# Kernel tuning notes

Hardware: AMD Instinct MI355X
Metric: run time of the kernel (lower is better)

The kernel has to match this reference:

```python
import jax, jax.numpy as jnp
import numpy as np

B, T, C, H, D, E, K = 4, 1024, 1024, 16, 64, 8, 2
HID = 2 * D  # expert MLP hidden width (assumed 2*head_dim)
NEG = jnp.finfo(jnp.float32).min


def setup_inputs() -> dict:
    key = jax.random.key(0)
    ks = jax.random.split(key, 16)
    s = 0.02
    # rotary tables [max_pos, head_dim]
    inv_freq = 1.0 / (10000.0 ** (jnp.arange(0, D, 2, dtype=jnp.float32) / D))
    freqs = jnp.arange(T, dtype=jnp.float32)[:, None] * inv_freq[None, :]
    emb = jnp.concatenate([freqs, freqs], axis=-1)  # [T, D]
    return {
        "x": jax.random.normal(ks[0], (B, T, C), jnp.float32),
        "position_ids": jnp.sort(jax.random.randint(ks[1], (B, T), 0, T), axis=-1),
        "cos": jnp.cos(emb),
        "sin": jnp.sin(emb),
        "rq": s * jax.random.normal(ks[2], (D, E), jnp.float32),
        "rk": s * jax.random.normal(ks[3], (D, E), jnp.float32),
        "rv": s * jax.random.normal(ks[4], (D, E), jnp.float32),
        "q_w1": s * jax.random.normal(ks[5], (E, D, HID), jnp.float32),
        "q_w2": s * jax.random.normal(ks[6], (E, HID, D), jnp.float32),
        "k_w1": s * jax.random.normal(ks[7], (E, D, HID), jnp.float32),
        "k_w2": s * jax.random.normal(ks[8], (E, HID, D), jnp.float32),
        "v_w1": s * jax.random.normal(ks[9], (E, D, HID), jnp.float32),
        "v_w2": s * jax.random.normal(ks[10], (E, HID, D), jnp.float32),
        "o_w": s * jax.random.normal(ks[11], (C, C), jnp.float32),  # torch Linear weight [out,in]
    }


def _rotate_half(x):
    x1, x2 = x[..., : D // 2], x[..., D // 2:]
    return jnp.concatenate([-x2, x1], axis=-1)


def _moe_head_proj(xh, r_w, w1, w2):
    """Per-head top-k routed expert MLP. xh: [B,T,H,D]."""
    logits = jnp.einsum('bthd,de->bthe', xh, r_w)            # router logits
    vals, idx = jax.lax.top_k(logits, K)                     # [B,T,H,K]
    w = jax.nn.softmax(vals, axis=-1)
    onehot = jax.nn.one_hot(idx, E, dtype=xh.dtype)          # [B,T,H,K,E]
    w_full = jnp.einsum('bthk,bthke->bthe', w, onehot)       # scatter weights to all experts
    h = jax.nn.gelu(jnp.einsum('bthd,edf->bthef', xh, w1))   # all-expert hidden
    out = jnp.einsum('bthe,bthef,efg->bthg', w_full, h, w2)  # masked weighted combine
    return out, logits


def reference(x, position_ids, cos, sin, rq, rk, rv, q_w1, q_w2, k_w1, k_w2, v_w1, v_w2, o_w):
    xh = x.reshape(B, T, H, D)
    q, _ = _moe_head_proj(xh, rq, q_w1, q_w2)
    k, _ = _moe_head_proj(xh, rk, k_w1, k_w2)
    v, _ = _moe_head_proj(xh, rv, v_w1, v_w2)
    q = q.transpose(0, 2, 1, 3)  # [B,H,T,D]
    k = k.transpose(0, 2, 1, 3)
    v = v.transpose(0, 2, 1, 3)
    # RoPE
    c = cos[position_ids][:, None, :, :]  # [B,1,T,D]
    s = sin[position_ids][:, None, :, :]
    q = q * c + _rotate_half(q) * s
    k = k * c + _rotate_half(k) * s
    # causal SDPA
    scores = jnp.einsum('bhqd,bhkd->bhqk', q, k) / jnp.sqrt(jnp.float32(D))
    causal = jnp.tril(jnp.ones((T, T), dtype=bool))
    scores = jnp.where(causal, scores, NEG)
    attn = jax.nn.softmax(scores, axis=-1)
    out = jnp.einsum('bhqk,bhkd->bhqd', attn, v)
    out = out.transpose(0, 2, 1, 3).reshape(B, T, C)
    return out @ o_w.T
```

## Files before the change

kernel.cpp:

```cpp
#include <hip/hip_runtime.h>
#include <math.h>

#define BB 4
#define TT 1024
#define CCH 1024
#define HH 16
#define DD 64
#define EE 8
#define HID 128
#define CAP 8192
#define GEXP 252

typedef unsigned short u16;
typedef short bf16x8 __attribute__((ext_vector_type(8)));
typedef float f32x4 __attribute__((ext_vector_type(4)));

__device__ __forceinline__ u16 f2bf(float f) {
    unsigned int u = __float_as_uint(f);
    unsigned int r = (u + 0x7FFFu + ((u >> 16) & 1u)) >> 16;
    return (u16)r;
}
__device__ __forceinline__ u16 f2bf_f(float f) {
    return (u16)((__float_as_uint(f) + 0x8000u) >> 16);
}
__device__ __forceinline__ float gelu_fast(float z) {
    float t = z * z;
    float wn = __builtin_fmaf(t, -0.07135481283f, -1.5957691216f);
    float e = __expf(z * wn);
    return __fdividef(z, 1.f + e);
}

__global__ __launch_bounds__(256) void router_kernel(
    const float* __restrict__ x,
    const float* __restrict__ rq, const float* __restrict__ rk, const float* __restrict__ rv,
    unsigned int* __restrict__ counts,
    unsigned int* __restrict__ idxbuf, float2* __restrict__ wtbuf)
{
    const int tid = threadIdx.x;
    const unsigned int g = blockIdx.x * 256 + tid;

    __shared__ float rS[3][64][8];
    __shared__ int lcnt[192];
    __shared__ int lbase[192];

    for (int i = tid; i < 1536; i += 256) {
        int p = i >> 9, rem = i & 511;
        const float* rp = (p == 0) ? rq : (p == 1) ? rk : rv;
        rS[p][rem >> 3][rem & 7] = rp[rem];
    }
    if (tid < 192) lcnt[tid] = 0;
    __syncthreads();

    float lg[3][8];
    #pragma unroll
    for (int p = 0; p < 3; ++p)
        #pragma unroll
        for (int e = 0; e < 8; ++e) lg[p][e] = 0.f;

    const float* xr = x + (size_t)g * 64;
    for (int i4 = 0; i4 < 16; ++i4) {
        float4 xv = ((const float4*)xr)[i4];
        float xa[4] = {xv.x, xv.y, xv.z, xv.w};
        #pragma unroll
        for (int m = 0; m < 4; ++m) {
            int d = i4 * 4 + m;
            #pragma unroll
            for (int p = 0; p < 3; ++p) {
                float4 r0 = *(const float4*)&rS[p][d][0];
                float4 r1 = *(const float4*)&rS[p][d][4];
                lg[p][0] += xa[m] * r0.x; lg[p][1] += xa[m] * r0.y;
                lg[p][2] += xa[m] * r0.z; lg[p][3] += xa[m] * r0.w;
                lg[p][4] += xa[m] * r1.x; lg[p][5] += xa[m] * r1.y;
                lg[p][6] += xa[m] * r1.z; lg[p][7] += xa[m] * r1.w;
            }
        }
    }

    int ppe[3]; float2 pw[3]; int slot[3];
    #pragma unroll
    for (int p = 0; p < 3; ++p) {
        int i1 = 0; float v1 = lg[p][0];
        #pragma unroll
        for (int e = 1; e < 8; ++e) { if (lg[p][e] > v1) { v1 = lg[p][e]; i1 = e; } }
        int i2 = -1; float v2 = -3.402823466e38f;
        #pragma unroll
        for (int e = 0; e < 8; ++e) { if (e != i1 && lg[p][e] > v2) { v2 = lg[p][e]; i2 = e; } }
        float z = __expf(v2 - v1);
        float inv = 1.f / (1.f + z);
        float wa = inv, wb = z * inv;
        int lo = min(i1, i2), hi = max(i1, i2);
        float wlo = (i1 < i2) ? wa : wb;
        float whi = (i1 < i2) ? wb : wa;
        int pel = p * 64 + lo * 8 + hi;
        ppe[p] = pel; pw[p] = make_float2(wlo, whi);
        slot[p] = atomicAdd(&lcnt[pel], 1);
    }
    __syncthreads();
    if (tid < 192) {
        int c = lcnt[tid];
        lbase[tid] = c ? (int)atomicAdd(&counts[tid], (unsigned int)c) : 0;
    }
    __syncthreads();
    #pragma unroll
    for (int p = 0; p < 3; ++p) {
        int pos = lbase[ppe[p]] + slot[p];
        if (pos < CAP) {
            idxbuf[ppe[p] * CAP + pos] = g;
            wtbuf[ppe[p] * CAP + pos]  = pw[p];
        }
    }
}

__global__ __launch_bounds__(128) void sched_kernel(
    const unsigned int* __restrict__ counts, unsigned int* __restrict__ blockinfo)
{
    const int tid = threadIdx.x;
    __shared__ int nsub[84];
    __shared__ int extra[84];
    __shared__ int frac[84];
    __shared__ int alloc[84];
    __shared__ int startS[84];
    __shared__ int nnzS, totalS, rem2S;

    if (tid < 84) {
        int p = tid / 28, q = tid - 28 * p, lo = 0;
        while (q >= 7 - lo) { q -= 7 - lo; ++lo; }
        int hi = lo + 1 + q;
        int n = (int)counts[p * 64 + lo * 8 + hi];
        if (n > CAP) n = CAP;
        nsub[tid] = (n + 31) >> 5;
    }
    __syncthreads();
    if (tid == 0) {
        int tot = 0, nz = 0;
        for (int i = 0; i < 84; ++i) { tot += nsub[i]; nz += (nsub[i] > 0); }
        totalS = tot; nnzS = nz;
    }
    __syncthreads();
    const int R = GEXP - nnzS;
    if (tid < 84) {
        if (nsub[tid] > 0) {
            int e = (int)(((long long)nsub[tid] * R) / totalS);
            extra[tid] = e;
            frac[tid] = nsub[tid] * R - e * totalS;
        } else { extra[tid] = 0; frac[tid] = -1; }
    }
    __syncthreads();
    if (tid == 0) {
        int se = 0;
        for (int i = 0; i < 84; ++i) se += extra[i];
        rem2S = GEXP - nnzS - se;
    }
    __syncthreads();
    if (tid < 84) {
        if (nsub[tid] > 0) {
            int rank = 0;
            for (int j = 0; j < 84; ++j)
                if (nsub[j] > 0 && (frac[j] > frac[tid] || (frac[j] == frac[tid] && j < tid))) ++rank;
            alloc[tid] = 1 + extra[tid] + (rank < rem2S ? 1 : 0);
        } else alloc[tid] = 0;
    }
    __syncthreads();
    if (tid == 0) {
        int s = 0;
        for (int i = 0; i < 84; ++i) { startS[i] = s; s += alloc[i]; }
    }
    __syncthreads();
    if (tid < 84) {
        int a = alloc[tid], st = startS[tid];
        for (int c = 0; c < a; ++c)
            blockinfo[st + c] = (unsigned)tid | ((unsigned)c << 8) | ((unsigned)a << 20);
    }
}

__global__ __launch_bounds__(768) void expert_kernel(
    const float* __restrict__ x, const int* __restrict__ pos_ids,
    const float* __restrict__ cosb, const float* __restrict__ sinb,
    const float* __restrict__ w1q, const float* __restrict__ w2q,
    const float* __restrict__ w1k, const float* __restrict__ w2k,
    const float* __restrict__ w1v, const float* __restrict__ w2v,
    const unsigned int* __restrict__ counts,
    const unsigned int* __restrict__ idxbuf, const float2* __restrict__ wtbuf,
    const unsigned int* __restrict__ blockinfo,
    u16* __restrict__ qb, u16* __restrict__ kb, u16* __restrict__ vb)
{
    const int tid = threadIdx.x;
    const unsigned int info = blockinfo[blockIdx.x];
    const int pe84 = info & 255;
    const int chunk = (info >> 8) & 0xFFF;
    const int nch = info >> 20;
    const int p = pe84 / 28;
    int q28 = pe84 - p * 28;
    int lo = 0;
    while (q28 >= 7 - lo) { q28 -= 7 - lo; ++lo; }
    const int hi = lo + 1 + q28;
    const int pe = p * 64 + lo * 8 + hi;

    int n = (int)counts[pe]; if (n == 0) return; if (n > CAP) n = CAP;

    const float* w1base = (p == 0) ? w1q : (p == 1) ? w1k : w1v;
    const float* w2base = (p == 0) ? w2q : (p == 1) ? w2k : w2v;
    u16* outp = (p == 0) ? qb : (p == 1) ? kb : vb;
    const unsigned int* il = idxbuf + pe * CAP;
    const float2* wl = wtbuf + pe * CAP;

    __shared__ u16 w1t[2][128][72];
    __shared__ u16 w2t[2][64][136];
    __shared__ u16 hsw[12][32][40];

    #pragma unroll
    for (int e = 0; e < 2; ++e) {
        int ex = e ? hi : lo;
        const float* w1 = w1base + ex * 64 * 128;
        const float* w2 = w2base + ex * 128 * 64;
        for (int i = tid; i < 8192; i += 768)
            w1t[e][i & 127][i >> 7] = f2bf(w1[i]);
        for (int i = tid; i < 8192; i += 768)
            w2t[e][i & 63][i >> 6] = f2bf(w2[i]);
    }
    __syncthreads();

    const int lane = tid & 63, w = tid >> 6, quad = lane >> 4, m16 = lane & 15;
    const int wid = chunk * 12 + w;
    const int WRK = nch * 12;
    const int nsub = (n + 31) >> 5;

    for (int s = wid; s < nsub; s += WRK) {
        const int base = s * 32;
        unsigned int gtok = 0, obase = 0; float wlo_ = 0.f, whi_ = 0.f;
        int posv = 0, valid = 0;
        if (lane < 32) {
            int j = base + lane;
            valid = (j < n);
            int jc = valid ? j : (n - 1);
            gtok = il[jc];
            float2 wv = wl[jc];
            wlo_ = valid ? wv.x : 0.f; whi_ = valid ? wv.y : 0.f;
            unsigned int b_ = gtok >> 14, h_ = gtok & 15, t_ = (gtok >> 4) & 1023;
            obase = ((b_ * 16 + h_) * 1024 + t_) * 64;
            posv = pos_ids[b_ * 1024 + t_];
        }

        bf16x8 Afr[2][2];
        #pragma unroll
        for (int mt2 = 0; mt2 < 2; ++mt2) {
            unsigned int gm = (unsigned int)__shfl((int)gtok, mt2 * 16 + m16, 64);
            const float* xr = x + (size_t)gm * 64 + 8 * quad;
            float4 xa0 = *(const float4*)(xr);
            float4 xa1 = *(const float4*)(xr + 4);
            float4 xb0 = *(const float4*)(xr + 32);
            float4 xb1 = *(const float4*)(xr + 36);
            bf16x8 A0, A1;
            A0[0] = (short)f2bf_f(xa0.x); A0[1] = (short)f2bf_f(xa0.y);
            A0[2] = (short)f2bf_f(xa0.z); A0[3] = (short)f2bf_f(xa0.w);
            A0[4] = (short)f2bf_f(xa1.x); A0[5] = (short)f2bf_f(xa1.y);
            A0[6] = (short)f2bf_f(xa1.z); A0[7] = (short)f2bf_f(xa1.w);
            A1[0] = (short)f2bf_f(xb0.x); A1[1] = (short)f2bf_f(xb0.y);
            A1[2] = (short)f2bf_f(xb0.z); A1[3] = (short)f2bf_f(xb0.w);
            A1[4] = (short)f2bf_f(xb1.x); A1[5] = (short)f2bf_f(xb1.y);
            A1[6] = (short)f2bf_f(xb1.z); A1[7] = (short)f2bf_f(xb1.w);
            Afr[mt2][0] = A0; Afr[mt2][1] = A1;
        }

        f32x4 acc2[2][2][4];
        #pragma unroll
        for (int e = 0; e < 2; ++e)
            #pragma unroll
            for (int mt2 = 0; mt2 < 2; ++mt2)
                #pragma unroll
                for (int nt = 0; nt < 4; ++nt) acc2[e][mt2][nt] = (f32x4){0.f, 0.f, 0.f, 0.f};

        #pragma unroll
        for (int e = 0; e < 2; ++e) {
            #pragma unroll
            for (int kk = 0; kk < 4; ++kk) {
                int nt0 = 2 * kk, nt1 = 2 * kk + 1;
                bf16x8 b0a = *(const bf16x8*)&w1t[e][16 * nt0 + m16][8 * quad];
                bf16x8 b0b = *(const bf16x8*)&w1t[e][16 * nt0 + m16][32 + 8 * quad];
                bf16x8 b1a = *(const bf16x8*)&w1t[e][16 * nt1 + m16][8 * quad];
                bf16x8 b1b = *(const bf16x8*)&w1t[e][16 * nt1 + m16][32 + 8 * quad];
                #pragma unroll
                for (int mt2 = 0; mt2 < 2; ++mt2) {
                    f32x4 c0 = (f32x4){0.f, 0.f, 0.f, 0.f};
                    f32x4 c1 = (f32x4){0.f, 0.f, 0.f, 0.f};
                    c0 = __builtin_amdgcn_mfma_f32_16x16x32_bf16(Afr[mt2][0], b0a, c0, 0, 0, 0);
                    c0 = __builtin_amdgcn_mfma_f32_16x16x32_bf16(Afr[mt2][1], b0b, c0, 0, 0, 0);
                    c1 = __builtin_amdgcn_mfma_f32_16x16x32_bf16(Afr[mt2][0], b1a, c1, 0, 0, 0);
                    c1 = __builtin_amdgcn_mfma_f32_16x16x32_bf16(Afr[mt2][1], b1b, c1, 0, 0, 0);
                    #pragma unroll
                    for (int r = 0; r < 4; ++r) {
                        hsw[w][mt2 * 16 + 4 * quad + r][m16]      = f2bf_f(gelu_fast(c0[r]));
                        hsw[w][mt2 * 16 + 4 * quad + r][16 + m16] = f2bf_f(gelu_fast(c1[r]));
                    }
                }
                bf16x8 A2_0 = *(const bf16x8*)&hsw[w][m16][8 * quad];
                bf16x8 A2_1 = *(const bf16x8*)&hsw[w][16 + m16][8 * quad];
                #pragma unroll
                for (int nt2 = 0; nt2 < 4; ++nt2) {
                    bf16x8 b2 = *(const bf16x8*)&w2t[e][16 * nt2 + m16][32 * kk + 8 * quad];
                    acc2[e][0][nt2] = __builtin_amdgcn_mfma_f32_16x16x32_bf16(A2_0, b2, acc2[e][0][nt2], 0, 0, 0);
                    acc2[e][1][nt2] = __builtin_amdgcn_mfma_f32_16x16x32_bf16(A2_1, b2, acc2[e][1][nt2], 0, 0, 0);
                }
            }
        }

        #pragma unroll
        for (int mt2 = 0; mt2 < 2; ++mt2) {
            #pragma unroll
            for (int r = 0; r < 4; ++r) {
                int tk = mt2 * 16 + 4 * quad + r;
                float wlo_r = __shfl(wlo_, tk, 64);
                float whi_r = __shfl(whi_, tk, 64);
                int   pos_r = __shfl(posv, tk, 64);
                unsigned int ob = (unsigned int)__shfl((int)obase, tk, 64);
                int   val_r = __shfl(valid, tk, 64);
                if (p < 2) {
                    #pragma unroll
                    for (int ntp = 0; ntp < 2; ++ntp) {
                        int d = 16 * ntp + m16;
                        float v1 = wlo_r * acc2[0][mt2][ntp][r]     + whi_r * acc2[1][mt2][ntp][r];
                        float v2 = wlo_r * acc2[0][mt2][ntp + 2][r] + whi_r * acc2[1][mt2][ntp + 2][r];
                        float cd = cosb[pos_r * 64 + d];
                        float sd = sinb[pos_r * 64 + d];
                        if (val_r) {
                            outp[ob + d]      = f2bf(v1 * cd - v2 * sd);
                            outp[ob + d + 32] = f2bf(v2 * cd + v1 * sd);
                        }
                    }
                } else {
                    #pragma unroll
                    for (int nt = 0; nt < 4; ++nt) {
                        float v = wlo_r * acc2[0][mt2][nt][r] + whi_r * acc2[1][mt2][nt][r];
                        if (val_r) outp[ob + 16 * nt + m16] = f2bf(v);
                    }
                }
            }
        }
    }
}

__global__ __launch_bounds__(256) void cvt_bf16_kernel(
    const float* __restrict__ in, u16* __restrict__ out, int n4)
{
    int i = blockIdx.x * 256 + threadIdx.x;
    if (i >= n4) return;
    float4 v = ((const float4*)in)[i];
    unsigned int lov = (unsigned int)f2bf(v.x) | ((unsigned int)f2bf(v.y) << 16);
    unsigned int hiv = (unsigned int)f2bf(v.z) | ((unsigned int)f2bf(v.w) << 16);
    ((uint2*)out)[i] = make_uint2(lov, hiv);
}

__global__ __launch_bounds__(256) void attn_kernel(
    const u16* __restrict__ qbp, const u16* __restrict__ kbp,
    const u16* __restrict__ vbp, u16* __restrict__ ao)
{
    const int tid = threadIdx.x;
    const int i8 = blockIdx.x & 7;
    const int plane_i = blockIdx.x >> 3;
    const int h = plane_i & 15, b = plane_i >> 4;
    const size_t plane = (size_t)plane_i * 1024 * 64;
    const u16* qp = qbp + plane;
    const u16* kp = kbp + plane;
    const u16* vp = vbp + plane;

    const int w = tid >> 6, lane = tid & 63, quad = lane >> 4, m16 = lane & 15;
    const int row = tid >> 2, seg = tid & 3;
    const int kjv = tid & 63, dgv = tid >> 6;

    __shared__ u16 Ks[64][72];
    __shared__ u16 Vt[64][72];
    __shared__ u16 Ps[4][16][72];

    #pragma unroll 1
    for (int half = 0; half < 2; ++half) {
        const int qt = half ? (15 - i8) : i8;
        const int q0 = qt * 64;

        const u16* qrow = &qp[(size_t)(q0 + 16 * w + m16) * 64 + 8 * quad];
        bf16x8 aq0 = *(const bf16x8*)(qrow);
        bf16x8 aq1 = *(const bf16x8*)(qrow + 32);

        uint4 kr0, kr1; ushort4 vr0, vr1, vr2, vr3;
        {
            const uint4* src = (const uint4*)&kp[(size_t)row * 64 + seg * 16];
            kr0 = src[0]; kr1 = src[1];
            const u16* vb2 = &vp[(size_t)kjv * 64 + dgv * 4];
            vr0 = *(const ushort4*)(vb2);
            vr1 = *(const ushort4*)(vb2 + 16);
            vr2 = *(const ushort4*)(vb2 + 32);
            vr3 = *(const ushort4*)(vb2 + 48);
        }

        float m_r[4], l_r[4];
        #pragma unroll
        for (int i = 0; i < 4; ++i) { m_r[i] = -1e30f; l_r[i] = 0.f; }
        f32x4 oacc[4];
        #pragma unroll
        for (int i = 0; i < 4; ++i) oacc[i] = (f32x4){0.f, 0.f, 0.f, 0.f};

        for (int kt = 0; kt <= qt; ++kt) {
            __syncthreads();
            {
                uint4* dst = (uint4*)&Ks[row][seg * 16];
                dst[0] = kr0; dst[1] = kr1;
                int d0 = dgv * 4;
                Vt[d0 + 0][kjv] = vr0.x; Vt[d0 + 1][kjv] = vr0.y;
                Vt[d0 + 2][kjv] = vr0.z; Vt[d0 + 3][kjv] = vr0.w;
                Vt[d0 + 16][kjv] = vr1.x; Vt[d0 + 17][kjv] = vr1.y;
                Vt[d0 + 18][kjv] = vr1.z; Vt[d0 + 19][kjv] = vr1.w;
                Vt[d0 + 32][kjv] = vr2.x; Vt[d0 + 33][kjv] = vr2.y;
                Vt[d0 + 34][kjv] = vr2.z; Vt[d0 + 35][kjv] = vr2.w;
                Vt[d0 + 48][kjv] = vr3.x; Vt[d0 + 49][kjv] = vr3.y;
                Vt[d0 + 50][kjv] = vr3.z; Vt[d0 + 51][kjv] = vr3.w;
            }
            __syncthreads();
            if (kt < qt) {
                const int k0n = (kt + 1) * 64;
                const uint4* src = (const uint4*)&kp[(size_t)(k0n + row) * 64 + seg * 16];
                kr0 = src[0]; kr1 = src[1];
                const u16* vb2 = &vp[(size_t)(k0n + kjv) * 64 + dgv * 4];
                vr0 = *(const ushort4*)(vb2);
                vr1 = *(const ushort4*)(vb2 + 16);
                vr2 = *(const ushort4*)(vb2 + 32);
                vr3 = *(const ushort4*)(vb2 + 48);
            }

            f32x4 sv[4];
            #pragma unroll
            for (int ct = 0; ct < 4; ++ct) {
                bf16x8 bk0 = *(const bf16x8*)&Ks[16 * ct + m16][8 * quad];
                bf16x8 bk1 = *(const bf16x8*)&Ks[16 * ct + m16][32 + 8 * quad];
                f32x4 acc = (f32x4){0.f, 0.f, 0.f, 0.f};
                acc = __builtin_amdgcn_mfma_f32_16x16x32_bf16(aq0, bk0, acc, 0, 0, 0);
                acc = __builtin_amdgcn_mfma_f32_16x16x32_bf16(aq1, bk1, acc, 0, 0, 0);
                sv[ct] = acc;
            }

            float s[4][4];
            const bool diag = (kt == qt);
            #pragma unroll
            for (int ct = 0; ct < 4; ++ct)
                #pragma unroll
                for (int reg = 0; reg < 4; ++reg) {
                    float v = sv[ct][reg] * 0.125f;
                    if (diag) {
                        int col = 16 * ct + m16;
                        int rw = 16 * w + 4 * quad + reg;
                        if (col > rw) v = -1e30f;
                    }
                    s[ct][reg] = v;
                }

            float nm[4], al[4];
            #pragma unroll
            for (int reg = 0; reg < 4; ++reg) {
                float rm = fmaxf(fmaxf(s[0][reg], s[1][reg]), fmaxf(s[2][reg], s[3][reg]));
                #pragma unroll
                for (int off = 1; off < 16; off <<= 1) rm = fmaxf(rm, __shfl_xor(rm, off, 16));
                float mn = fmaxf(m_r[reg], rm);
                nm[reg] = mn;
                al[reg] = __expf(m_r[reg] - mn);
            }
            #pragma unroll
            for (int reg = 0; reg < 4; ++reg) {
                float sum = 0.f;
                #pragma unroll
                for (int ct = 0; ct < 4; ++ct) {
                    float pv = __expf(s[ct][reg] - nm[reg]);
                    s[ct][reg] = pv;
                    sum += pv;
                }
                #pragma unroll
                for (int off = 1; off < 16; off <<= 1) sum += __shfl_xor(sum, off, 16);
                l_r[reg] = l_r[reg] * al[reg] + sum;
                m_r[reg] = nm[reg];
            }

            #pragma unroll
            for (int ct = 0; ct < 4; ++ct)
                #pragma unroll
                for (int reg = 0; reg < 4; ++reg)
                    Ps[w][4 * quad + reg][16 * ct + m16] = f2bf(s[ct][reg]);

            #pragma unroll
            for (int dt = 0; dt < 4; ++dt)
                #pragma unroll
                for (int reg = 0; reg < 4; ++reg) oacc[dt][reg] *= al[reg];

            bf16x8 ap0 = *(const bf16x8*)&Ps[w][m16][8 * quad];
            bf16x8 ap1 = *(const bf16x8*)&Ps[w][m16][32 + 8 * quad];
            #pragma unroll
            for (int dt = 0; dt < 4; ++dt) {
                bf16x8 bv0 = *(const bf16x8*)&Vt[16 * dt + m16][8 * quad];
                bf16x8 bv1 = *(const bf16x8*)&Vt[16 * dt + m16][32 + 8 * quad];
                oacc[dt] = __builtin_amdgcn_mfma_f32_16x16x32_bf16(ap0, bv0, oacc[dt], 0, 0, 0);
                oacc[dt] = __builtin_amdgcn_mfma_f32_16x16x32_bf16(ap1, bv1, oacc[dt], 0, 0, 0);
            }
        }

        #pragma unroll
        for (int reg = 0; reg < 4; ++reg) {
            float linv = 1.f / l_r[reg];
            int rw = q0 + 16 * w + 4 * quad + reg;
            size_t base = ((size_t)(b * 1024) + rw) * 1024 + h * 64;
            #pragma unroll
            for (int dt = 0; dt < 4; ++dt)
                ao[base + 16 * dt + m16] = f2bf(oacc[dt][reg] * linv);
        }
    }
}

__global__ __launch_bounds__(256) void oproj_kernel(
    const u16* __restrict__ A, const u16* __restrict__ Bw,
    float* __restrict__ out)
{
    const int tid = threadIdx.x;
    const int bn = blockIdx.x & 7;
    const int bm = blockIdx.x >> 3;
    const int m0 = bm * 128, n0 = bn * 128;
    const int w = tid >> 6, lane = tid & 63, quad = lane >> 4, m16 = lane & 15;
    const int wm = (w >> 1) * 64, wn = (w & 1) * 64;

    __shared__ u16 As[128][32];
    __shared__ u16 Bs[128][32];

    f32x4 acc[4][4];
    #pragma unroll
    for (int mt = 0; mt < 4; ++mt)
        #pragma unroll
        for (int nt = 0; nt < 4; ++nt) acc[mt][nt] = (f32x4){0.f, 0.f, 0.f, 0.f};

    for (int k0 = 0; k0 < 1024; k0 += 32) {
        __syncthreads();
        {
            int rw = tid >> 1, sg = (tid & 1) * 16;
            const uint4* srcA = (const uint4*)&A[(size_t)(m0 + rw) * 1024 + k0 + sg];
            uint4 a0 = srcA[0], a1 = srcA[1];
            uint4* dstA = (uint4*)&As[rw][sg];
            dstA[0] = a0; dstA[1] = a1;
            const uint4* srcB = (const uint4*)&Bw[(size_t)(n0 + rw) * 1024 + k0 + sg];
            uint4 b0 = srcB[0], b1 = srcB[1];
            uint4* dstB = (uint4*)&Bs[rw][sg];
            dstB[0] = b0; dstB[1] = b1;
        }
        __syncthreads();
        bf16x8 af[4], bf_[4];
        #pragma unroll
        for (int mt = 0; mt < 4; ++mt) af[mt] = *(const bf16x8*)&As[wm + 16 * mt + m16][8 * quad];
        #pragma unroll
        for (int nt = 0; nt < 4; ++nt) bf_[nt] = *(const bf16x8*)&Bs[wn + 16 * nt + m16][8 * quad];
        #pragma unroll
        for (int mt = 0; mt < 4; ++mt)
            #pragma unroll
            for (int nt = 0; nt < 4; ++nt)
                acc[mt][nt] = __builtin_amdgcn_mfma_f32_16x16x32_bf16(af[mt], bf_[nt], acc[mt][nt], 0, 0, 0);
    }
    #pragma unroll
    for (int mt = 0; mt < 4; ++mt)
        #pragma unroll
        for (int nt = 0; nt < 4; ++nt)
            #pragma unroll
            for (int reg = 0; reg < 4; ++reg)
                out[(size_t)(m0 + wm + 16 * mt + 4 * quad + reg) * 1024 + n0 + wn + 16 * nt + m16] =
                    acc[mt][nt][reg];
}

extern "C" void kernel_launch(void* const* d_in, const int* in_sizes, int n_in,
                              void* d_out, int out_size, void* d_ws, size_t ws_size,
                              hipStream_t stream) {
    (void)in_sizes; (void)n_in; (void)out_size; (void)ws_size;
    const float* x    = (const float*)d_in[0];
    const int*   pid  = (const int*)  d_in[1];
    const float* cosb = (const float*)d_in[2];
    const float* sinb = (const float*)d_in[3];
    const float* rq   = (const float*)d_in[4];
    const float* rk   = (const float*)d_in[5];
    const float* rv   = (const float*)d_in[6];
    const float* qw1  = (const float*)d_in[7];
    const float* qw2  = (const float*)d_in[8];
    const float* kw1  = (const float*)d_in[9];
    const float* kw2  = (const float*)d_in[10];
    const float* vw1  = (const float*)d_in[11];
    const float* vw2  = (const float*)d_in[12];
    const float* ow   = (const float*)d_in[13];
    float* out = (float*)d_out;

    const size_t MB = 1u << 20;
    char* wsb = (char*)d_ws;
    u16* qb   = (u16*)(wsb + 0 * MB);
    u16* kb   = (u16*)(wsb + 8 * MB);
    u16* vb   = (u16*)(wsb + 16 * MB);
    u16* aobf = (u16*)(wsb + 24 * MB);
    u16* owbf = (u16*)(wsb + 32 * MB);
    unsigned int* idxbuf = (unsigned int*)(wsb + 34 * MB);
    float2*       wtbuf  = (float2*)(wsb + 41 * MB);
    unsigned int* counts = (unsigned int*)(wsb + 54 * MB);
    unsigned int* blockinfo = (unsigned int*)(wsb + 54 * MB + 4096);

    hipMemsetAsync(counts, 0, 1024, stream);

    hipLaunchKernelGGL(router_kernel, dim3(256), dim3(256), 0, stream,
                       x, rq, rk, rv, counts, idxbuf, wtbuf);
    hipLaunchKernelGGL(sched_kernel, dim3(1), dim3(128), 0, stream,
                       counts, blockinfo);
    hipLaunchKernelGGL(cvt_bf16_kernel, dim3(1024), dim3(256), 0, stream,
                       ow, owbf, 1024 * 1024 / 4);
    hipLaunchKernelGGL(expert_kernel, dim3(GEXP), dim3(768), 0, stream,
                       x, pid, cosb, sinb, qw1, qw2, kw1, kw2, vw1, vw2,
                       counts, idxbuf, wtbuf, blockinfo, qb, kb, vb);
    hipLaunchKernelGGL(attn_kernel, dim3(512), dim3(256), 0, stream,
                       qb, kb, vb, aobf);
    hipLaunchKernelGGL(oproj_kernel, dim3(256), dim3(256), 0, stream,
                       aobf, owbf, out);
}
```

Baseline: 257.0 us.

## Pre-swizzle bf16 expert weights and keep MoE hidden activations in registers

A new kernel converts the expert W1/W2 weights once into XOR-swizzled bf16 images. The expert kernel then copies them straight into LDS with global_load_lds instead of doing a per-block fp32 convert and transpose. The GELU hidden tile now moves between the two MFMA stages through lane shuffles instead of an LDS round trip. Routing weights are folded into the hidden activations so both experts share one accumulator set. Block size drops to 512 threads and the grid doubles, which adds one extra kernel launch and makes the result depend on the scheduler's handling of the larger grid.

```diff
diff --git a/kernel.cpp b/kernel.cpp
--- a/kernel.cpp
+++ b/kernel.cpp
@@ -9,9 +9,10 @@
 #define EE 8
 #define HID 128
 #define CAP 8192
-#define GEXP 252
+#define GEXP 504
 
 typedef unsigned short u16;
+typedef unsigned int u32;
 typedef short bf16x8 __attribute__((ext_vector_type(8)));
 typedef float f32x4 __attribute__((ext_vector_type(4)));
 
@@ -22,6 +23,11 @@
 }
 __device__ __forceinline__ u16 f2bf_f(float f) {
     return (u16)((__float_as_uint(f) + 0x8000u) >> 16);
+}
+__device__ __forceinline__ u32 pkbf(float lo, float hi) {
+    u32 a = __float_as_uint(lo) + 0x8000u;
+    u32 b = __float_as_uint(hi) + 0x8000u;
+    return __builtin_amdgcn_perm(b, a, 0x07060302u);
 }
 __device__ __forceinline__ float gelu_fast(float z) {
     float t = z * z;
@@ -29,6 +35,10 @@
     float e = __expf(z * wn);
     return __fdividef(z, 1.f + e);
 }
+
+#define GLD16(gp, lp) __builtin_amdgcn_global_load_lds( \
+    (const __attribute__((address_space(1))) u32*)(gp), \
+    (__attribute__((address_space(3))) u32*)(lp), 16, 0, 0)
 
 __global__ __launch_bounds__(256) void router_kernel(
     const float* __restrict__ x,
@@ -173,12 +183,45 @@
     }
 }
 
-__global__ __launch_bounds__(768) void expert_kernel(
+__global__ __launch_bounds__(256) void wcvt_kernel(
+    const float* __restrict__ qw1, const float* __restrict__ kw1, const float* __restrict__ vw1,
+    const float* __restrict__ qw2, const float* __restrict__ kw2, const float* __restrict__ vw2,
+    u16* __restrict__ img1, u16* __restrict__ img2)
+{
+    int t = blockIdx.x * 256 + threadIdx.x;
+    u16 tmp[8];
+    if (t < 24576) {
+        int c = t & 7, f = (t >> 3) & 127, e = (t >> 10) & 7, p = t >> 13;
+        const float* w1 = ((p == 0) ? qw1 : (p == 1) ? kw1 : vw1) + e * 8192;
+        int dbase = 8 * (c ^ (f & 7));
+        #pragma unroll
+        for (int j = 0; j < 8; ++j) tmp[j] = f2bf(w1[(dbase + j) * 128 + f]);
+        uint4 ov;
+        ov.x = (u32)tmp[0] | ((u32)tmp[1] << 16);
+        ov.y = (u32)tmp[2] | ((u32)tmp[3] << 16);
+        ov.z = (u32)tmp[4] | ((u32)tmp[5] << 16);
+        ov.w = (u32)tmp[6] | ((u32)tmp[7] << 16);
+        ((uint4*)img1)[t] = ov;
+    } else {
+        int i = t - 24576;
+        int c = i & 15, g = (i >> 4) & 63, e = (i >> 10) & 7, p = i >> 13;
+        const float* w2 = ((p == 0) ? qw2 : (p == 1) ? kw2 : vw2) + e * 8192;
+        int fbase = 8 * (c ^ (g & 15));
+        #pragma unroll
+        for (int j = 0; j < 8; ++j) tmp[j] = f2bf(w2[(fbase + j) * 64 + g]);
+        uint4 ov;
+        ov.x = (u32)tmp[0] | ((u32)tmp[1] << 16);
+        ov.y = (u32)tmp[2] | ((u32)tmp[3] << 16);
+        ov.z = (u32)tmp[4] | ((u32)tmp[5] << 16);
+        ov.w = (u32)tmp[6] | ((u32)tmp[7] << 16);
+        ((uint4*)img2)[i] = ov;
+    }
+}
+
+__global__ __launch_bounds__(512, 4) void expert_kernel(
     const float* __restrict__ x, const int* __restrict__ pos_ids,
     const float* __restrict__ cosb, const float* __restrict__ sinb,
-    const float* __restrict__ w1q, const float* __restrict__ w2q,
-    const float* __restrict__ w1k, const float* __restrict__ w2k,
-    const float* __restrict__ w1v, const float* __restrict__ w2v,
+    const u16* __restrict__ img1, const u16* __restrict__ img2,
     const unsigned int* __restrict__ counts,
     const unsigned int* __restrict__ idxbuf, const float2* __restrict__ wtbuf,
     const unsigned int* __restrict__ blockinfo,
@@ -198,31 +241,34 @@
 
     int n = (int)counts[pe]; if (n == 0) return; if (n > CAP) n = CAP;
 
-    const float* w1base = (p == 0) ? w1q : (p == 1) ? w1k : w1v;
-    const float* w2base = (p == 0) ? w2q : (p == 1) ? w2k : w2v;
     u16* outp = (p == 0) ? qb : (p == 1) ? kb : vb;
     const unsigned int* il = idxbuf + pe * CAP;
     const float2* wl = wtbuf + pe * CAP;
 
-    __shared__ u16 w1t[2][128][72];
-    __shared__ u16 w2t[2][64][136];
-    __shared__ u16 hsw[12][32][40];
-
-    #pragma unroll
-    for (int e = 0; e < 2; ++e) {
-        int ex = e ? hi : lo;
-        const float* w1 = w1base + ex * 64 * 128;
-        const float* w2 = w2base + ex * 128 * 64;
-        for (int i = tid; i < 8192; i += 768)
-            w1t[e][i & 127][i >> 7] = f2bf(w1[i]);
-        for (int i = tid; i < 8192; i += 768)
-            w2t[e][i & 63][i >> 6] = f2bf(w2[i]);
+    __shared__ __align__(16) u16 wsh[32768];
+
+    {
+        const u16* a0 = img1 + (p * 8 + lo) * 8192;
+        const u16* b0 = img2 + (p * 8 + lo) * 8192;
+        const u16* a1 = img1 + (p * 8 + hi) * 8192;
+        const u16* b1 = img2 + (p * 8 + hi) * 8192;
+        #pragma unroll
+        for (int k = 0; k < 2; ++k) {
+            int o = (k * 512 + tid) * 8;
+            GLD16(a0 + o, wsh + o);
+            GLD16(b0 + o, wsh + 8192 + o);
+            GLD16(a1 + o, wsh + 16384 + o);
+            GLD16(b1 + o, wsh + 24576 + o);
+        }
     }
     __syncthreads();
 
     const int lane = tid & 63, w = tid >> 6, quad = lane >> 4, m16 = lane & 15;
-    const int wid = chunk * 12 + w;
-    const int WRK = nch * 12;
+    const int f7 = m16 & 7;
+    const int sA = m16 + ((quad & 1) << 5);
+    const int sB = sA + 16;
+    const int wid = chunk * 8 + w;
+    const int WRK = nch * 8;
     const int nsub = (n + 31) >> 5;
 
     for (int s = wid; s < nsub; s += WRK) {
@@ -240,6 +286,11 @@
             obase = ((b_ * 16 + h_) * 1024 + t_) * 64;
             posv = pos_ids[b_ * 1024 + t_];
         }
+
+        float wf00 = __shfl(wlo_, m16, 64);
+        float wf10 = __shfl(whi_, m16, 64);
+        float wf01 = __shfl(wlo_, 16 + m16, 64);
+        float wf11 = __shfl(whi_, 16 + m16, 64);
 
         bf16x8 Afr[2][2];
         #pragma unroll
@@ -262,44 +313,71 @@
             Afr[mt2][0] = A0; Afr[mt2][1] = A1;
         }
 
-        f32x4 acc2[2][2][4];
-        #pragma unroll
-        for (int e = 0; e < 2; ++e)
-            #pragma unroll
-            for (int mt2 = 0; mt2 < 2; ++mt2)
-                #pragma unroll
-                for (int nt = 0; nt < 4; ++nt) acc2[e][mt2][nt] = (f32x4){0.f, 0.f, 0.f, 0.f};
+        f32x4 acc2[2][4];
+        #pragma unroll
+        for (int mt2 = 0; mt2 < 2; ++mt2)
+            #pragma unroll
+            for (int nt = 0; nt < 4; ++nt) acc2[mt2][nt] = (f32x4){0.f, 0.f, 0.f, 0.f};
 
         #pragma unroll
         for (int e = 0; e < 2; ++e) {
+            const u16* w1b = wsh + e * 16384;
+            const u16* w2b = w1b + 8192;
+            const float wt0 = e ? wf10 : wf00;
+            const float wt1 = e ? wf11 : wf01;
             #pragma unroll
             for (int kk = 0; kk < 4; ++kk) {
-                int nt0 = 2 * kk, nt1 = 2 * kk + 1;
-                bf16x8 b0a = *(const bf16x8*)&w1t[e][16 * nt0 + m16][8 * quad];
-                bf16x8 b0b = *(const bf16x8*)&w1t[e][16 * nt0 + m16][32 + 8 * quad];
-                bf16x8 b1a = *(const bf16x8*)&w1t[e][16 * nt1 + m16][8 * quad];
-                bf16x8 b1b = *(const bf16x8*)&w1t[e][16 * nt1 + m16][32 + 8 * quad];
-                #pragma unroll
-                for (int mt2 = 0; mt2 < 2; ++mt2) {
-                    f32x4 c0 = (f32x4){0.f, 0.f, 0.f, 0.f};
-                    f32x4 c1 = (f32x4){0.f, 0.f, 0.f, 0.f};
-                    c0 = __builtin_amdgcn_mfma_f32_16x16x32_bf16(Afr[mt2][0], b0a, c0, 0, 0, 0);
-                    c0 = __builtin_amdgcn_mfma_f32_16x16x32_bf16(Afr[mt2][1], b0b, c0, 0, 0, 0);
-                    c1 = __builtin_amdgcn_mfma_f32_16x16x32_bf16(Afr[mt2][0], b1a, c1, 0, 0, 0);
-                    c1 = __builtin_amdgcn_mfma_f32_16x16x32_bf16(Afr[mt2][1], b1b, c1, 0, 0, 0);
+                f32x4 c[2][2];
+                #pragma unroll
+                for (int ntl = 0; ntl < 2; ++ntl) {
+                    const int f = 16 * (2 * kk + ntl) + m16;
+                    const u16* w1f = w1b + f * 64;
+                    bf16x8 wa = *(const bf16x8*)(w1f + (((quad    ) ^ f7) << 3));
+                    bf16x8 wb = *(const bf16x8*)(w1f + (((quad + 4) ^ f7) << 3));
                     #pragma unroll
-                    for (int r = 0; r < 4; ++r) {
-                        hsw[w][mt2 * 16 + 4 * quad + r][m16]      = f2bf_f(gelu_fast(c0[r]));
-                        hsw[w][mt2 * 16 + 4 * quad + r][16 + m16] = f2bf_f(gelu_fast(c1[r]));
+                    for (int mt2 = 0; mt2 < 2; ++mt2) {
+                        f32x4 t = (f32x4){0.f, 0.f, 0.f, 0.f};
+                        t = __builtin_amdgcn_mfma_f32_16x16x32_bf16(wa, Afr[mt2][0], t, 0, 0, 0);
+                        c[ntl][mt2] = __builtin_amdgcn_mfma_f32_16x16x32_bf16(wb, Afr[mt2][1], t, 0, 0, 0);
                     }
                 }
-                bf16x8 A2_0 = *(const bf16x8*)&hsw[w][m16][8 * quad];
-                bf16x8 A2_1 = *(const bf16x8*)&hsw[w][16 + m16][8 * quad];
-                #pragma unroll
-                for (int nt2 = 0; nt2 < 4; ++nt2) {
-                    bf16x8 b2 = *(const bf16x8*)&w2t[e][16 * nt2 + m16][32 * kk + 8 * quad];
-                    acc2[e][0][nt2] = __builtin_amdgcn_mfma_f32_16x16x32_bf16(A2_0, b2, acc2[e][0][nt2], 0, 0, 0);
-                    acc2[e][1][nt2] = __builtin_amdgcn_mfma_f32_16x16x32_bf16(A2_1, b2, acc2[e][1][nt2], 0, 0, 0);
+                const int c2base = (((4 * kk + quad) ^ m16) << 3);
+                #pragma unroll
+                for (int mt2 = 0; mt2 < 2; ++mt2) {
+                    const float wt = mt2 ? wt1 : wt0;
+                    u32 pl0, ph0, pl1, ph1;
+                    {
+                        float g0 = wt * gelu_fast(c[0][mt2][0]);
+                        float g1 = wt * gelu_fast(c[0][mt2][1]);
+                        float g2 = wt * gelu_fast(c[0][mt2][2]);
+                        float g3 = wt * gelu_fast(c[0][mt2][3]);
+                        pl0 = pkbf(g0, g1); ph0 = pkbf(g2, g3);
+                        g0 = wt * gelu_fast(c[1][mt2][0]);
+                        g1 = wt * gelu_fast(c[1][mt2][1]);
+                        g2 = wt * gelu_fast(c[1][mt2][2]);
+                        g3 = wt * gelu_fast(c[1][mt2][3]);
+                        pl1 = pkbf(g0, g1); ph1 = pkbf(g2, g3);
+                    }
+                    u32 q0l = (u32)__shfl((int)pl0, sA, 64);
+                    u32 q1l = (u32)__shfl((int)pl1, sA, 64);
+                    u32 q0h = (u32)__shfl((int)ph0, sA, 64);
+                    u32 q1h = (u32)__shfl((int)ph1, sA, 64);
+                    u32 r0l = (u32)__shfl((int)pl0, sB, 64);
+                    u32 r1l = (u32)__shfl((int)pl1, sB, 64);
+                    u32 r0h = (u32)__shfl((int)ph0, sB, 64);
+                    u32 r1h = (u32)__shfl((int)ph1, sB, 64);
+                    const bool hisel = (quad & 2);
+                    union { u32 u[4]; bf16x8 v; } a2;
+                    a2.u[0] = hisel ? q1l : q0l;
+                    a2.u[1] = hisel ? q1h : q0h;
+                    a2.u[2] = hisel ? r1l : r0l;
+                    a2.u[3] = hisel ? r1h : r0h;
+                    #pragma unroll
+                    for (int nt2 = 0; nt2 < 4; ++nt2) {
+                        const u16* w2f = w2b + (16 * nt2 + m16) * 128 + c2base;
+                        bf16x8 b2 = *(const bf16x8*)w2f;
+                        acc2[mt2][nt2] = __builtin_amdgcn_mfma_f32_16x16x32_bf16(a2.v, b2, acc2[mt2][nt2], 0, 0, 0);
+                    }
                 }
             }
         }
@@ -309,8 +387,6 @@
             #pragma unroll
             for (int r = 0; r < 4; ++r) {
                 int tk = mt2 * 16 + 4 * quad + r;
-                float wlo_r = __shfl(wlo_, tk, 64);
-                float whi_r = __shfl(whi_, tk, 64);
                 int   pos_r = __shfl(posv, tk, 64);
                 unsigned int ob = (unsigned int)__shfl((int)obase, tk, 64);
                 int   val_r = __shfl(valid, tk, 64);
@@ -318,8 +394,8 @@
                     #pragma unroll
                     for (int ntp = 0; ntp < 2; ++ntp) {
                         int d = 16 * ntp + m16;
-                        float v1 = wlo_r * acc2[0][mt2][ntp][r]     + whi_r * acc2[1][mt2][ntp][r];
-                        float v2 = wlo_r * acc2[0][mt2][ntp + 2][r] + whi_r * acc2[1][mt2][ntp + 2][r];
+                        float v1 = acc2[mt2][ntp][r];
+                        float v2 = acc2[mt2][ntp + 2][r];
                         float cd = cosb[pos_r * 64 + d];
                         float sd = sinb[pos_r * 64 + d];
                         if (val_r) {
@@ -330,7 +406,7 @@
                 } else {
                     #pragma unroll
                     for (int nt = 0; nt < 4; ++nt) {
-                        float v = wlo_r * acc2[0][mt2][nt][r] + whi_r * acc2[1][mt2][nt][r];
+                        float v = acc2[mt2][nt][r];
                         if (val_r) outp[ob + 16 * nt + m16] = f2bf(v);
                     }
                 }
@@ -596,17 +672,21 @@
     float2*       wtbuf  = (float2*)(wsb + 41 * MB);
     unsigned int* counts = (unsigned int*)(wsb + 54 * MB);
     unsigned int* blockinfo = (unsigned int*)(wsb + 54 * MB + 4096);
+    u16* w1img = (u16*)(wsb + 56 * MB);
+    u16* w2img = (u16*)(wsb + 57 * MB);
 
     hipMemsetAsync(counts, 0, 1024, stream);
 
+    hipLaunchKernelGGL(wcvt_kernel, dim3(192), dim3(256), 0, stream,
+                       qw1, kw1, vw1, qw2, kw2, vw2, w1img, w2img);
     hipLaunchKernelGGL(router_kernel, dim3(256), dim3(256), 0, stream,
                        x, rq, rk, rv, counts, idxbuf, wtbuf);
     hipLaunchKernelGGL(sched_kernel, dim3(1), dim3(128), 0, stream,
                        counts, blockinfo);
     hipLaunchKernelGGL(cvt_bf16_kernel, dim3(1024), dim3(256), 0, stream,
                        ow, owbf, 1024 * 1024 / 4);
-    hipLaunchKernelGGL(expert_kernel, dim3(GEXP), dim3(768), 0, stream,
-                       x, pid, cosb, sinb, qw1, qw2, kw1, kw2, vw1, vw2,
+    hipLaunchKernelGGL(expert_kernel, dim3(GEXP), dim3(512), 0, stream,
+                       x, pid, cosb, sinb, w1img, w2img,
                        counts, idxbuf, wtbuf, blockinfo, qb, kb, vb);
     hipLaunchKernelGGL(attn_kernel, dim3(512), dim3(256), 0, stream,
                        qb, kb, vb, aobf);
```

Result: slower. 367.2 us (+42.9%).
